# Performance work log

Measured on AMD Instinct MI355X. Metric: run time of the kernel, lower is better.

The kernel has to match this reference:

```python
import jax, jax.numpy as jnp
import numpy as np

EMBED_DIM = 512
FFN_DIM = 64
N_QUBITS = 16
BATCH = 16
SEQ = 4096


def setup_inputs() -> dict:
    key = jax.random.key(0)
    ks = jax.random.split(key, 6)
    x = jax.random.normal(ks[0], (BATCH, SEQ, EMBED_DIM), dtype=jnp.float32)
    theta = jax.random.normal(ks[1], (N_QUBITS,), dtype=jnp.float32)
    W1 = jax.random.normal(ks[2], (FFN_DIM, N_QUBITS), dtype=jnp.float32) * (1.0 / np.sqrt(N_QUBITS))
    b1 = jax.random.normal(ks[3], (FFN_DIM,), dtype=jnp.float32) * 0.02
    W2 = jax.random.normal(ks[4], (EMBED_DIM, FFN_DIM), dtype=jnp.float32) * (1.0 / np.sqrt(FFN_DIM))
    b2 = jax.random.normal(ks[5], (EMBED_DIM,), dtype=jnp.float32) * 0.02
    return {"x": x, "theta": theta, "W1": W1, "b1": b1, "W2": W2, "b2": b2}


def reference(x, theta, W1, b1, W2, b2):
    # Quantum circuit closed form: per wire i, |0> -> RX(x_i) -> RY(theta_i),
    # <PauliZ> = cos(x_i) * cos(theta_i). Only the first n_qubits features of x are encoded.
    z = jnp.cos(x[..., :N_QUBITS]) * jnp.cos(theta)              # [B, S, Q]
    h = jnp.einsum('bsq,fq->bsf', z, W1) + b1                    # [B, S, F] (dropout is identity at eval)
    out = jnp.einsum('bsf,ef->bse', jax.nn.relu(h), W2) + b2     # [B, S, E]
    return out
```

## Files before the change

### kernel.cpp

```cpp
#include <hip/hip_runtime.h>
#include <hip/hip_bf16.h>


#define EMBED 512
#define FFN   64
#define NQ    16
#define ROWS  65536
#define ROWS_PER_BLOCK 128
#define MITERS (ROWS_PER_BLOCK / 16)
#define NBLOCKS (ROWS / ROWS_PER_BLOCK)

typedef __attribute__((ext_vector_type(8))) short short8;
typedef __attribute__((ext_vector_type(4))) short short4_t;
typedef __attribute__((ext_vector_type(4))) float floatx4;

__device__ __forceinline__ short f2bf(float f) {
    union { float f; unsigned u; } v; v.f = f;
    unsigned u = v.u;
    unsigned r = (u + 0x7fffu + ((u >> 16) & 1u)) >> 16;
    return (short)r;
}

__global__ __launch_bounds__(256, 2)
void ffq_kernel(const float* __restrict__ x,
                const float* __restrict__ theta,
                const float* __restrict__ W1,
                const float* __restrict__ b1,
                const float* __restrict__ W2,
                const float* __restrict__ b2,
                float* __restrict__ out)
{
    __shared__ __align__(16) float w1_s[FFN][NQ];
    __shared__ __align__(16) float z_s[2][16][20];
    __shared__ __align__(16) short h_s[2][16][72];

    const int t    = threadIdx.x;
    const int lane = t & 63;
    const int w    = t >> 6;
    const int quad = lane >> 4;
    const int l16  = lane & 15;

    ((float4*)&w1_s[0][0])[t] = ((const float4*)W1)[t];

    const float cth = cosf(theta[t & 15]);
    const float4 b1v = ((const float4*)b1)[t >> 4];
    float b1a[4] = {b1v.x, b1v.y, b1v.z, b1v.w};

    float b2r[8];
#pragma unroll
    for (int tile = 0; tile < 8; ++tile)
        b2r[tile] = b2[w * 128 + tile * 16 + l16];

    short8 bfrag[8][2];
#pragma unroll
    for (int tile = 0; tile < 8; ++tile) {
        const int e = w * 128 + tile * 16 + l16;
#pragma unroll
        for (int s = 0; s < 2; ++s) {
            const int f0 = s * 32 + quad * 8;
            const float4* p = (const float4*)(W2 + (size_t)e * FFN + f0);
            float4 lo = p[0], hi = p[1];
            short8 bfr;
            bfr[0] = f2bf(lo.x); bfr[1] = f2bf(lo.y); bfr[2] = f2bf(lo.z); bfr[3] = f2bf(lo.w);
            bfr[4] = f2bf(hi.x); bfr[5] = f2bf(hi.y); bfr[6] = f2bf(hi.z); bfr[7] = f2bf(hi.w);
            bfrag[tile][s] = bfr;
        }
    }

    const int rowBase = blockIdx.x * ROWS_PER_BLOCK;

    for (int it = 0; it < MITERS; ++it) {
        const int buf  = it & 1;
        const int row0 = rowBase + it * 16;

        {
            const int zr = t >> 4, zq = t & 15;
            const float xv = x[(size_t)(row0 + zr) * EMBED + zq];
            z_s[buf][zr][zq] = cosf(xv) * cth;
        }
        __syncthreads();

        {
            const int r = t & 15, g = t >> 4;
            const float4 zr0 = *(const float4*)&z_s[buf][r][0];
            const float4 zr1 = *(const float4*)&z_s[buf][r][4];
            const float4 zr2 = *(const float4*)&z_s[buf][r][8];
            const float4 zr3 = *(const float4*)&z_s[buf][r][12];
            short4_t hv;
#pragma unroll
            for (int i = 0; i < 4; ++i) {
                const float4* wr = (const float4*)&w1_s[g * 4 + i][0];
                const float4 w0 = wr[0], w1r = wr[1], w2r = wr[2], w3r = wr[3];
                float s0 = b1a[i];
                s0 += zr0.x * w0.x  + zr0.y * w0.y  + zr0.z * w0.z  + zr0.w * w0.w;
                s0 += zr1.x * w1r.x + zr1.y * w1r.y + zr1.z * w1r.z + zr1.w * w1r.w;
                s0 += zr2.x * w2r.x + zr2.y * w2r.y + zr2.z * w2r.z + zr2.w * w2r.w;
                s0 += zr3.x * w3r.x + zr3.y * w3r.y + zr3.z * w3r.z + zr3.w * w3r.w;
                s0 = fmaxf(s0, 0.0f);
                hv[i] = f2bf(s0);
            }
            *(short4_t*)&h_s[buf][r][g * 4] = hv;
        }
        __syncthreads();

        const short8 a0 = *(const short8*)&h_s[buf][l16][quad * 8];
        const short8 a1 = *(const short8*)&h_s[buf][l16][32 + quad * 8];

#pragma unroll
        for (int tile = 0; tile < 8; ++tile) {
            floatx4 acc = {0.f, 0.f, 0.f, 0.f};
            acc = __builtin_amdgcn_mfma_f32_16x16x32_bf16(a0, bfrag[tile][0], acc, 0, 0, 0);
            acc = __builtin_amdgcn_mfma_f32_16x16x32_bf16(a1, bfrag[tile][1], acc, 0, 0, 0);

            const int e = w * 128 + tile * 16 + l16;
#pragma unroll
            for (int reg = 0; reg < 4; ++reg) {
                const int r = row0 + quad * 4 + reg;
                out[(size_t)r * EMBED + e] = acc[reg] + b2r[tile];
            }
        }
    }
}

extern "C" void kernel_launch(void* const* d_in, const int* in_sizes, int n_in,
                              void* d_out, int out_size, void* d_ws, size_t ws_size,
                              hipStream_t stream) {
    const float* x     = (const float*)d_in[0];
    const float* theta = (const float*)d_in[1];
    const float* W1    = (const float*)d_in[2];
    const float* b1    = (const float*)d_in[3];
    const float* W2    = (const float*)d_in[4];
    const float* b2    = (const float*)d_in[5];
    float* out = (float*)d_out;

    ffq_kernel<<<NBLOCKS, 256, 0, stream>>>(x, theta, W1, b1, W2, b2, out);
}
```

Baseline: 226.8 us.

## Swap MFMA operands for vectorized stores and batch all rows per block

The MFMA operands are swapped so W2 is the A operand and h is the B operand. Each lane then holds four consecutive output columns and writes them with one float4 store instead of four strided scalar stores. The 8-iteration loop with two barriers per iteration is replaced by one up-front phase: all 128 rows of x are loaded as float4, cos and the first layer are computed for every row with W1 held in registers, and only two barriers are used. Bias b2 now seeds the accumulator. The cost is higher register use and larger shared buffers, which could reduce occupancy.

```diff
diff --git a/kernel.cpp b/kernel.cpp
--- a/kernel.cpp
+++ b/kernel.cpp
@@ -1,14 +1,10 @@
 #include <hip/hip_runtime.h>
-#include <hip/hip_bf16.h>
 
 
 #define EMBED 512
 #define FFN   64
-#define NQ    16
-#define ROWS  65536
-#define ROWS_PER_BLOCK 128
-#define MITERS (ROWS_PER_BLOCK / 16)
-#define NBLOCKS (ROWS / ROWS_PER_BLOCK)
+#define RPB   128
+#define NBLOCKS 512
 
 typedef __attribute__((ext_vector_type(8))) short short8;
 typedef __attribute__((ext_vector_type(4))) short short4_t;
@@ -17,8 +13,7 @@
 __device__ __forceinline__ short f2bf(float f) {
     union { float f; unsigned u; } v; v.f = f;
     unsigned u = v.u;
-    unsigned r = (u + 0x7fffu + ((u >> 16) & 1u)) >> 16;
-    return (short)r;
+    return (short)((u + 0x7fffu + ((u >> 16) & 1u)) >> 16);
 }
 
 __global__ __launch_bounds__(256, 2)
@@ -30,28 +25,25 @@
                 const float* __restrict__ b2,
                 float* __restrict__ out)
 {
-    __shared__ __align__(16) float w1_s[FFN][NQ];
-    __shared__ __align__(16) float z_s[2][16][20];
-    __shared__ __align__(16) short h_s[2][16][72];
+    __shared__ __align__(16) float z_s[RPB][20];
+    __shared__ __align__(16) short h_s[RPB][72];
 
     const int t    = threadIdx.x;
     const int lane = t & 63;
     const int w    = t >> 6;
     const int quad = lane >> 4;
     const int l16  = lane & 15;
+    const int rowBase = blockIdx.x * RPB;
 
-    ((float4*)&w1_s[0][0])[t] = ((const float4*)W1)[t];
+    const int c  = t & 3;
+    const int r0 = t >> 2;
+    const float4 xv0 = *(const float4*)(x + (size_t)(rowBase + r0)      * EMBED + c * 4);
+    const float4 xv1 = *(const float4*)(x + (size_t)(rowBase + r0 + 64) * EMBED + c * 4);
 
-    const float cth = cosf(theta[t & 15]);
-    const float4 b1v = ((const float4*)b1)[t >> 4];
-    float b1a[4] = {b1v.x, b1v.y, b1v.z, b1v.w};
+    const float4 th = *(const float4*)(theta + c * 4);
+    const float ctx = cosf(th.x), cty = cosf(th.y), ctz = cosf(th.z), ctw = cosf(th.w);
 
-    float b2r[8];
-#pragma unroll
-    for (int tile = 0; tile < 8; ++tile)
-        b2r[tile] = b2[w * 128 + tile * 16 + l16];
-
-    short8 bfrag[8][2];
+    short8 afrag[8][2];
 #pragma unroll
     for (int tile = 0; tile < 8; ++tile) {
         const int e = w * 128 + tile * 16 + l16;
@@ -59,65 +51,76 @@
         for (int s = 0; s < 2; ++s) {
             const int f0 = s * 32 + quad * 8;
             const float4* p = (const float4*)(W2 + (size_t)e * FFN + f0);
-            float4 lo = p[0], hi = p[1];
-            short8 bfr;
-            bfr[0] = f2bf(lo.x); bfr[1] = f2bf(lo.y); bfr[2] = f2bf(lo.z); bfr[3] = f2bf(lo.w);
-            bfr[4] = f2bf(hi.x); bfr[5] = f2bf(hi.y); bfr[6] = f2bf(hi.z); bfr[7] = f2bf(hi.w);
-            bfrag[tile][s] = bfr;
+            const float4 lo = p[0], hi = p[1];
+            short8 fr;
+            fr[0] = f2bf(lo.x); fr[1] = f2bf(lo.y); fr[2] = f2bf(lo.z); fr[3] = f2bf(lo.w);
+            fr[4] = f2bf(hi.x); fr[5] = f2bf(hi.y); fr[6] = f2bf(hi.z); fr[7] = f2bf(hi.w);
+            afrag[tile][s] = fr;
         }
     }
 
-    const int rowBase = blockIdx.x * ROWS_PER_BLOCK;
+    floatx4 b2f[8];
+#pragma unroll
+    for (int tile = 0; tile < 8; ++tile) {
+        const float4 v = *(const float4*)(b2 + w * 128 + tile * 16 + quad * 4);
+        floatx4 a; a[0] = v.x; a[1] = v.y; a[2] = v.z; a[3] = v.w;
+        b2f[tile] = a;
+    }
 
-    for (int it = 0; it < MITERS; ++it) {
-        const int buf  = it & 1;
-        const int row0 = rowBase + it * 16;
+    const int g = t >> 4;
+    float4 w1r[4][4];
+#pragma unroll
+    for (int i = 0; i < 4; ++i)
+#pragma unroll
+        for (int kq = 0; kq < 4; ++kq)
+            w1r[i][kq] = *(const float4*)(W1 + (size_t)(g * 4 + i) * 16 + kq * 4);
+    const float4 b1v = *(const float4*)(b1 + g * 4);
+    float b1a[4] = {b1v.x, b1v.y, b1v.z, b1v.w};
 
-        {
-            const int zr = t >> 4, zq = t & 15;
-            const float xv = x[(size_t)(row0 + zr) * EMBED + zq];
-            z_s[buf][zr][zq] = cosf(xv) * cth;
+    {
+        float4 z0, z1;
+        z0.x = cosf(xv0.x) * ctx; z0.y = cosf(xv0.y) * cty;
+        z0.z = cosf(xv0.z) * ctz; z0.w = cosf(xv0.w) * ctw;
+        z1.x = cosf(xv1.x) * ctx; z1.y = cosf(xv1.y) * cty;
+        z1.z = cosf(xv1.z) * ctz; z1.w = cosf(xv1.w) * ctw;
+        *(float4*)&z_s[r0][c * 4]      = z0;
+        *(float4*)&z_s[r0 + 64][c * 4] = z1;
+    }
+    __syncthreads();
+
+    const int hr = t & 15;
+#pragma unroll
+    for (int rg = 0; rg < 8; ++rg) {
+        const int r = rg * 16 + hr;
+        const float4 zr0 = *(const float4*)&z_s[r][0];
+        const float4 zr1 = *(const float4*)&z_s[r][4];
+        const float4 zr2 = *(const float4*)&z_s[r][8];
+        const float4 zr3 = *(const float4*)&z_s[r][12];
+        short4_t hv;
+#pragma unroll
+        for (int i = 0; i < 4; ++i) {
+            float s0 = b1a[i];
+            s0 += zr0.x * w1r[i][0].x + zr0.y * w1r[i][0].y + zr0.z * w1r[i][0].z + zr0.w * w1r[i][0].w;
+            s0 += zr1.x * w1r[i][1].x + zr1.y * w1r[i][1].y + zr1.z * w1r[i][1].z + zr1.w * w1r[i][1].w;
+            s0 += zr2.x * w1r[i][2].x + zr2.y * w1r[i][2].y + zr2.z * w1r[i][2].z + zr2.w * w1r[i][2].w;
+            s0 += zr3.x * w1r[i][3].x + zr3.y * w1r[i][3].y + zr3.z * w1r[i][3].z + zr3.w * w1r[i][3].w;
+            hv[i] = f2bf(fmaxf(s0, 0.0f));
         }
-        __syncthreads();
+        *(short4_t*)&h_s[r][g * 4] = hv;
+    }
+    __syncthreads();
 
-        {
-            const int r = t & 15, g = t >> 4;
-            const float4 zr0 = *(const float4*)&z_s[buf][r][0];
-            const float4 zr1 = *(const float4*)&z_s[buf][r][4];
-            const float4 zr2 = *(const float4*)&z_s[buf][r][8];
-            const float4 zr3 = *(const float4*)&z_s[buf][r][12];
-            short4_t hv;
-#pragma unroll
-            for (int i = 0; i < 4; ++i) {
-                const float4* wr = (const float4*)&w1_s[g * 4 + i][0];
-                const float4 w0 = wr[0], w1r = wr[1], w2r = wr[2], w3r = wr[3];
-                float s0 = b1a[i];
-                s0 += zr0.x * w0.x  + zr0.y * w0.y  + zr0.z * w0.z  + zr0.w * w0.w;
-                s0 += zr1.x * w1r.x + zr1.y * w1r.y + zr1.z * w1r.z + zr1.w * w1r.w;
-                s0 += zr2.x * w2r.x + zr2.y * w2r.y + zr2.z * w2r.z + zr2.w * w2r.w;
-                s0 += zr3.x * w3r.x + zr3.y * w3r.y + zr3.z * w3r.z + zr3.w * w3r.w;
-                s0 = fmaxf(s0, 0.0f);
-                hv[i] = f2bf(s0);
-            }
-            *(short4_t*)&h_s[buf][r][g * 4] = hv;
-        }
-        __syncthreads();
-
-        const short8 a0 = *(const short8*)&h_s[buf][l16][quad * 8];
-        const short8 a1 = *(const short8*)&h_s[buf][l16][32 + quad * 8];
-
+#pragma unroll 2
+    for (int rg = 0; rg < 8; ++rg) {
+        const short8 hb0 = *(const short8*)&h_s[rg * 16 + l16][quad * 8];
+        const short8 hb1 = *(const short8*)&h_s[rg * 16 + l16][32 + quad * 8];
+        float* op = out + (size_t)(rowBase + rg * 16 + l16) * EMBED + w * 128 + quad * 4;
 #pragma unroll
         for (int tile = 0; tile < 8; ++tile) {
-            floatx4 acc = {0.f, 0.f, 0.f, 0.f};
-            acc = __builtin_amdgcn_mfma_f32_16x16x32_bf16(a0, bfrag[tile][0], acc, 0, 0, 0);
-            acc = __builtin_amdgcn_mfma_f32_16x16x32_bf16(a1, bfrag[tile][1], acc, 0, 0, 0);
-
-            const int e = w * 128 + tile * 16 + l16;
-#pragma unroll
-            for (int reg = 0; reg < 4; ++reg) {
-                const int r = row0 + quad * 4 + reg;
-                out[(size_t)r * EMBED + e] = acc[reg] + b2r[tile];
-            }
+            floatx4 acc = b2f[tile];
+            acc = __builtin_amdgcn_mfma_f32_16x16x32_bf16(afrag[tile][0], hb0, acc, 0, 0, 0);
+            acc = __builtin_amdgcn_mfma_f32_16x16x32_bf16(afrag[tile][1], hb1, acc, 0, 0, 0);
+            *(floatx4*)(op + tile * 16) = acc;
         }
     }
 }
```

New measurement: 230.5 us. Within noise of the previous version (+1.6%).
